# Kernel optimization log

Hardware: AMD Instinct MI355X
Metric: run time of the kernel (lower is better)

The kernel has to match this reference:

```python
import math
import jax, jax.numpy as jnp
import numpy as np

N_HEADS = 16
D_EMBED = 1024
D_HEAD = D_EMBED // N_HEADS
B, S = 4, 2048


def setup_inputs() -> dict:
    key = jax.random.key(0)
    k1, k2, k3, k4, k5 = jax.random.split(key, 5)
    scale_in = 1.0 / math.sqrt(D_EMBED)
    return {
        "x": jax.random.normal(k1, (B, S, D_EMBED), dtype=jnp.float32),
        "w_in": jax.random.normal(k2, (3 * D_EMBED, D_EMBED), dtype=jnp.float32) * scale_in,
        "b_in": jax.random.normal(k3, (3 * D_EMBED,), dtype=jnp.float32) * 0.02,
        "w_out": jax.random.normal(k4, (D_EMBED, D_EMBED), dtype=jnp.float32) * scale_in,
        "b_out": jax.random.normal(k5, (D_EMBED,), dtype=jnp.float32) * 0.02,
        "causal_mask": 1,
    }


def reference(x, w_in, b_in, w_out, b_out, causal_mask):
    Bn, Sn, D = x.shape
    # fused QKV projection (torch Linear: x @ W.T + b)
    qkv = x @ w_in.T + b_in                       # (B, S, 3D)
    q, k, v = jnp.split(qkv, 3, axis=-1)
    def to_heads(t):
        return t.reshape(Bn, Sn, N_HEADS, D_HEAD).transpose(0, 2, 1, 3)  # (B,H,S,dh)
    q, k, v = to_heads(q), to_heads(k), to_heads(v)
    # manual scaled dot-product attention, full (B,H,S,S) scores
    scores = jnp.einsum("bhqd,bhkd->bhqk", q, k)
    if causal_mask:
        tri = jnp.triu(jnp.ones((Sn, Sn), dtype=bool), k=1)
        scores = jnp.where(tri, -jnp.inf, scores)
    scores = scores / math.sqrt(D_HEAD)
    weights = jax.nn.softmax(scores, axis=-1)
    out = jnp.einsum("bhqk,bhkd->bhqd", weights, v)  # (B,H,S,dh)
    out = out.transpose(0, 2, 1, 3).reshape(Bn, Sn, D)
    return out @ w_out.T + b_out
```

## Files before the change

kernel.cpp:

```cpp
#include <hip/hip_runtime.h>

typedef __bf16 bf16x8 __attribute__((ext_vector_type(8)));
typedef float  f32x4  __attribute__((ext_vector_type(4)));
typedef unsigned int uint;

__device__ inline unsigned short f2bf(float f) {
  union { float f; unsigned int u; } v; v.f = f;
  unsigned int u = v.u;
  unsigned int r = u + 0x7FFF + ((u >> 16) & 1);
  return (unsigned short)(r >> 16);
}

__device__ inline uint pack_bf16_rhu(float a, float b) {
  uint ua = __builtin_bit_cast(uint, a) + 0x8000u;
  uint ub = __builtin_bit_cast(uint, b) + 0x8000u;
  return __builtin_amdgcn_perm(ub, ua, 0x07060302u);
}

__device__ inline void load_lds16(const unsigned short* g, unsigned short* l) {
  __builtin_amdgcn_global_load_lds(
      (const __attribute__((address_space(1))) uint*)(g),
      (__attribute__((address_space(3))) uint*)(l), 16, 0, 0);
}

__global__ void cvt_f32_bf16(const float* __restrict__ in,
                             unsigned short* __restrict__ out, int n) {
  int i = (blockIdx.x * blockDim.x + threadIdx.x) * 4;
  if (i + 3 < n) {
    float4 f = *reinterpret_cast<const float4*>(in + i);
    ushort4 o;
    o.x = f2bf(f.x); o.y = f2bf(f.y); o.z = f2bf(f.z); o.w = f2bf(f.w);
    *reinterpret_cast<ushort4*>(out + i) = o;
  } else {
    for (; i < n; ++i) out[i] = f2bf(in[i]);
  }
}

template<bool OUT_BF16>
__global__ __launch_bounds__(256) void gemm_bt128(
    const unsigned short* __restrict__ A,
    const unsigned short* __restrict__ B,
    const float* __restrict__ bias,
    void* __restrict__ Cout,
    int M, int N, int K, int ldc, float scale, int ncut)
{
  __shared__ __attribute__((aligned(16))) unsigned short As[128 * 64];
  __shared__ __attribute__((aligned(16))) unsigned short Bs[128 * 64];

  const int t    = threadIdx.x;
  const int wave = t >> 6, lane = t & 63;
  const int l16  = lane & 15, quad = lane >> 4;
  const int wr = wave >> 1, wc = wave & 1;
  const int m0 = blockIdx.y * 128, n0 = blockIdx.x * 128;

  f32x4 acc[4][4] = {};

  for (int k0 = 0; k0 < K; k0 += 64) {
#pragma unroll
    for (int i = 0; i < 4; ++i) {
      int chunk = i * 256 + t;
      int row = chunk >> 3, col = (chunk & 7) * 8;
      load_lds16(A + (size_t)(m0 + row) * K + k0 + col, As + chunk * 8);
    }
#pragma unroll
    for (int i = 0; i < 4; ++i) {
      int chunk = i * 256 + t;
      int row = chunk >> 3, col = (chunk & 7) * 8;
      load_lds16(B + (size_t)(n0 + row) * K + k0 + col, Bs + chunk * 8);
    }
    __syncthreads();
#pragma unroll
    for (int ks = 0; ks < 2; ++ks) {
      bf16x8 af[4], bfr[4];
#pragma unroll
      for (int mt = 0; mt < 4; ++mt)
        af[mt] = *(const bf16x8*)(As + (wr * 64 + mt * 16 + l16) * 64 + ks * 32 + quad * 8);
#pragma unroll
      for (int nt = 0; nt < 4; ++nt)
        bfr[nt] = *(const bf16x8*)(Bs + (wc * 64 + nt * 16 + l16) * 64 + ks * 32 + quad * 8);
#pragma unroll
      for (int mt = 0; mt < 4; ++mt)
#pragma unroll
        for (int nt = 0; nt < 4; ++nt)
          acc[mt][nt] = __builtin_amdgcn_mfma_f32_16x16x32_bf16(af[mt], bfr[nt], acc[mt][nt], 0, 0, 0);
    }
    __syncthreads();
  }

#pragma unroll
  for (int nt = 0; nt < 4; ++nt) {
    int col = n0 + wc * 64 + nt * 16 + l16;
    float bv = bias[col];
    float mlt = (col < ncut) ? scale : 1.0f;
#pragma unroll
    for (int mt = 0; mt < 4; ++mt) {
#pragma unroll
      for (int r = 0; r < 4; ++r) {
        int row = m0 + wr * 64 + mt * 16 + quad * 4 + r;
        float v = (acc[mt][nt][r] + bv) * mlt;
        if (OUT_BF16)
          ((unsigned short*)Cout)[(size_t)row * ldc + col] = f2bf(v);
        else
          ((float*)Cout)[(size_t)row * ldc + col] = v;
      }
    }
  }
}

__global__ __launch_bounds__(256) void attn(
    const unsigned short* __restrict__ qkv,
    unsigned short* __restrict__ y,
    const int* __restrict__ flag)
{
  __shared__ __attribute__((aligned(16))) unsigned short Qs[64][72];
  __shared__ __attribute__((aligned(16))) unsigned short Ks[64][72];
  __shared__ __attribute__((aligned(16))) unsigned short VtF[64 * 64];

  const int t    = threadIdx.x;
  const int wave = t >> 6, lane = t & 63;
  const int l16  = lane & 15, quad = lane >> 4;
  const int idx = blockIdx.x;
  const int bh  = idx & 63;
  const int qt  = 31 - (idx >> 6);
  const int b = bh >> 4, h = bh & 15;
  const int causal = flag[0];
  const int q0 = qt * 64;

  const unsigned short* Qg = qkv + (size_t)b * 2048 * 3072 + h * 64;
  const unsigned short* Kg = Qg + 1024;
  const unsigned short* Vg = Qg + 2048;

  {
    int r = t >> 2, c = (t & 3) * 16;
    const unsigned short* src = Qg + (size_t)(q0 + r) * 3072 + c;
    *(uint4*)&Qs[r][c]     = *(const uint4*)src;
    *(uint4*)&Qs[r][c + 8] = *(const uint4*)(src + 8);
  }
  __syncthreads();
  bf16x8 qf[2];
  qf[0] = *(const bf16x8*)&Qs[wave * 16 + l16][quad * 8];
  qf[1] = *(const bf16x8*)&Qs[wave * 16 + l16][32 + quad * 8];
  __syncthreads();
  unsigned short (*Ps)[72] = Qs;

  f32x4 ot[4] = {};
  float l_lane = 0.f;
  const int q_glob = q0 + wave * 16 + l16;
  const int jmax = causal ? qt : 31;
  const int h7 = ((l16 >> 3) + (l16 & 7)) & 7;

  const int kr = t >> 2, kc = (t & 3) * 16;
  const int vr = t >> 3, vg = t & 7, vc = vg * 8;
  const int bk0 = vr >> 3, r7 = vr & 7;

  uint4 kreg0, kreg1, vreg0, vreg1;
  {
    const unsigned short* src = Kg + (size_t)kr * 3072 + kc;
    kreg0 = *(const uint4*)src;
    kreg1 = *(const uint4*)(src + 8);
    vreg0 = *(const uint4*)(Vg + (size_t)vr * 3072 + vc);
    vreg1 = *(const uint4*)(Vg + (size_t)(vr + 32) * 3072 + vc);
  }

  for (int j = 0; j <= jmax; ++j) {
    *(uint4*)&Ks[kr][kc]     = kreg0;
    *(uint4*)&Ks[kr][kc + 8] = kreg1;
    {
      const unsigned short* vs0 = (const unsigned short*)&vreg0;
      const unsigned short* vs1 = (const unsigned short*)&vreg1;
#pragma unroll
      for (int i = 0; i < 8; ++i) {
        int d = vc + i;
        VtF[d * 64 + (((bk0     + vg + i) & 7) << 3) + r7] = vs0[i];
        VtF[d * 64 + (((bk0 + 4 + vg + i) & 7) << 3) + r7] = vs1[i];
      }
    }
    __syncthreads();

    if (j < jmax) {
      const int kvn = (j + 1) * 64;
      const unsigned short* src = Kg + (size_t)(kvn + kr) * 3072 + kc;
      kreg0 = *(const uint4*)src;
      kreg1 = *(const uint4*)(src + 8);
      vreg0 = *(const uint4*)(Vg + (size_t)(kvn + vr) * 3072 + vc);
      vreg1 = *(const uint4*)(Vg + (size_t)(kvn + vr + 32) * 3072 + vc);
    }

    f32x4 st[4] = {};
#pragma unroll
    for (int ks = 0; ks < 2; ++ks) {
#pragma unroll
      for (int mt = 0; mt < 4; ++mt) {
        bf16x8 kf = *(const bf16x8*)&Ks[mt * 16 + l16][ks * 32 + quad * 8];
        st[mt] = __builtin_amdgcn_mfma_f32_16x16x32_bf16(kf, qf[ks], st[mt], 0, 0, 0);
      }
    }

    const bool diag = (causal != 0) && (j == qt);
    const int kv0 = j * 64;
#pragma unroll
    for (int mt = 0; mt < 4; ++mt) {
      float p[4];
#pragma unroll
      for (int r = 0; r < 4; ++r) {
        float pv = __builtin_amdgcn_exp2f(st[mt][r]);
        if (diag) {
          int kv = kv0 + mt * 16 + quad * 4 + r;
          if (kv > q_glob) pv = 0.f;
        }
        p[r] = pv;
      }
      l_lane += (p[0] + p[1]) + (p[2] + p[3]);
      uint2 w;
      w.x = pack_bf16_rhu(p[0], p[1]);
      w.y = pack_bf16_rhu(p[2], p[3]);
      *(uint2*)&Ps[wave * 16 + l16][mt * 16 + quad * 4] = w;
    }
    __threadfence_block();

#pragma unroll
    for (int ks = 0; ks < 2; ++ks) {
      bf16x8 pf = *(const bf16x8*)&Ps[wave * 16 + l16][ks * 32 + quad * 8];
#pragma unroll
      for (int mt = 0; mt < 4; ++mt) {
        int blk = (ks * 4 + quad + 2 * mt + h7) & 7;
        bf16x8 vf = *(const bf16x8*)(VtF + (mt * 16 + l16) * 64 + (blk << 3));
        ot[mt] = __builtin_amdgcn_mfma_f32_16x16x32_bf16(vf, pf, ot[mt], 0, 0, 0);
      }
    }
    __syncthreads();
  }

  l_lane += __shfl_xor(l_lane, 16);
  l_lane += __shfl_xor(l_lane, 32);
  float inv = 1.f / l_lane;

#pragma unroll
  for (int mt = 0; mt < 4; ++mt) {
    uint2 w;
    w.x = pack_bf16_rhu(ot[mt][0] * inv, ot[mt][1] * inv);
    w.y = pack_bf16_rhu(ot[mt][2] * inv, ot[mt][3] * inv);
    *(uint2*)&Ps[wave * 16 + l16][mt * 16 + quad * 4] = w;
  }
  __syncthreads();
  {
    int r = t >> 2, c = (t & 3) * 16;
    size_t base = ((size_t)b * 2048 + q0 + r) * 1024 + h * 64 + c;
    *(uint4*)(y + base)     = *(const uint4*)&Ps[r][c];
    *(uint4*)(y + base + 8) = *(const uint4*)&Ps[r][c + 8];
  }
}

extern "C" void kernel_launch(void* const* d_in, const int* in_sizes, int n_in,
                              void* d_out, int out_size, void* d_ws, size_t ws_size,
                              hipStream_t stream) {
  const float* x     = (const float*)d_in[0];
  const float* w_in  = (const float*)d_in[1];
  const float* b_in  = (const float*)d_in[2];
  const float* w_out = (const float*)d_in[3];
  const float* b_out = (const float*)d_in[4];
  const int*   cmask = (const int*)d_in[5];

  char* ws = (char*)d_ws;
  unsigned short* x_bf     = (unsigned short*)(ws);
  unsigned short* w_in_bf  = (unsigned short*)(ws + 16777216);
  unsigned short* w_out_bf = (unsigned short*)(ws + 23068672);
  unsigned short* qkv_bf   = (unsigned short*)(ws + 25165824);
  unsigned short* y_bf     = (unsigned short*)(ws + 75497472);

  const int n1 = 8192 * 1024, n2 = 3072 * 1024, n3 = 1024 * 1024;
  cvt_f32_bf16<<<dim3((n1 / 4 + 255) / 256), 256, 0, stream>>>(x, x_bf, n1);
  cvt_f32_bf16<<<dim3((n2 / 4 + 255) / 256), 256, 0, stream>>>(w_in, w_in_bf, n2);
  cvt_f32_bf16<<<dim3((n3 / 4 + 255) / 256), 256, 0, stream>>>(w_out, w_out_bf, n3);

  gemm_bt128<true><<<dim3(24, 64), 256, 0, stream>>>(
      x_bf, w_in_bf, b_in, qkv_bf, 8192, 3072, 1024, 3072,
      0.18033688011112042f, 1024);

  attn<<<dim3(2048), 256, 0, stream>>>(qkv_bf, y_bf, cmask);

  gemm_bt128<false><<<dim3(8, 64), 256, 0, stream>>>(
      y_bf, w_out_bf, b_out, d_out, 8192, 1024, 1024, 1024, 1.0f, 0);
}
```

Measured before the change: 282.2 us.

## Fuse conversions, XOR-swizzle GEMM LDS tiles, pre-transpose V for attention

```diff
diff --git a/kernel.cpp b/kernel.cpp
--- a/kernel.cpp
+++ b/kernel.cpp
@@ -23,17 +23,23 @@
       (__attribute__((address_space(3))) uint*)(l), 16, 0, 0);
 }
 
-__global__ void cvt_f32_bf16(const float* __restrict__ in,
-                             unsigned short* __restrict__ out, int n) {
+__device__ inline void cvt4(const float* in, unsigned short* out) {
+  float4 f = *reinterpret_cast<const float4*>(in);
+  ushort4 o;
+  o.x = f2bf(f.x); o.y = f2bf(f.y); o.z = f2bf(f.z); o.w = f2bf(f.w);
+  *reinterpret_cast<ushort4*>(out) = o;
+}
+
+__global__ void cvt_all(const float* __restrict__ x, const float* __restrict__ w_in,
+                        const float* __restrict__ w_out,
+                        unsigned short* __restrict__ x_bf,
+                        unsigned short* __restrict__ w_in_bf,
+                        unsigned short* __restrict__ w_out_bf) {
+  const int n1 = 8192 * 1024, n2 = 3072 * 1024;
   int i = (blockIdx.x * blockDim.x + threadIdx.x) * 4;
-  if (i + 3 < n) {
-    float4 f = *reinterpret_cast<const float4*>(in + i);
-    ushort4 o;
-    o.x = f2bf(f.x); o.y = f2bf(f.y); o.z = f2bf(f.z); o.w = f2bf(f.w);
-    *reinterpret_cast<ushort4*>(out + i) = o;
-  } else {
-    for (; i < n; ++i) out[i] = f2bf(in[i]);
-  }
+  if (i < n1)            cvt4(x + i, x_bf + i);
+  else if (i < n1 + n2)  cvt4(w_in + (i - n1), w_in_bf + (i - n1));
+  else                   cvt4(w_out + (i - n1 - n2), w_out_bf + (i - n1 - n2));
 }
 
 template<bool OUT_BF16>
@@ -52,6 +58,7 @@
   const int l16  = lane & 15, quad = lane >> 4;
   const int wr = wave >> 1, wc = wave & 1;
   const int m0 = blockIdx.y * 128, n0 = blockIdx.x * 128;
+  const int l8 = l16 & 7;
 
   f32x4 acc[4][4] = {};
 
@@ -59,14 +66,16 @@
 #pragma unroll
     for (int i = 0; i < 4; ++i) {
       int chunk = i * 256 + t;
-      int row = chunk >> 3, col = (chunk & 7) * 8;
-      load_lds16(A + (size_t)(m0 + row) * K + k0 + col, As + chunk * 8);
+      int row = chunk >> 3, cb = chunk & 7;
+      int gcb = cb ^ (row & 7);
+      load_lds16(A + (size_t)(m0 + row) * K + k0 + gcb * 8, As + chunk * 8);
     }
 #pragma unroll
     for (int i = 0; i < 4; ++i) {
       int chunk = i * 256 + t;
-      int row = chunk >> 3, col = (chunk & 7) * 8;
-      load_lds16(B + (size_t)(n0 + row) * K + k0 + col, Bs + chunk * 8);
+      int row = chunk >> 3, cb = chunk & 7;
+      int gcb = cb ^ (row & 7);
+      load_lds16(B + (size_t)(n0 + row) * K + k0 + gcb * 8, Bs + chunk * 8);
     }
     __syncthreads();
 #pragma unroll
@@ -74,10 +83,12 @@
       bf16x8 af[4], bfr[4];
 #pragma unroll
       for (int mt = 0; mt < 4; ++mt)
-        af[mt] = *(const bf16x8*)(As + (wr * 64 + mt * 16 + l16) * 64 + ks * 32 + quad * 8);
+        af[mt] = *(const bf16x8*)(As + (wr * 64 + mt * 16 + l16) * 64 +
+                                  (((ks * 4 + quad) ^ l8) << 3));
 #pragma unroll
       for (int nt = 0; nt < 4; ++nt)
-        bfr[nt] = *(const bf16x8*)(Bs + (wc * 64 + nt * 16 + l16) * 64 + ks * 32 + quad * 8);
+        bfr[nt] = *(const bf16x8*)(Bs + (wc * 64 + nt * 16 + l16) * 64 +
+                                   (((ks * 4 + quad) ^ l8) << 3));
 #pragma unroll
       for (int mt = 0; mt < 4; ++mt)
 #pragma unroll
@@ -107,8 +118,33 @@
   }
 }
 
+__global__ __launch_bounds__(256) void vtrans(const unsigned short* __restrict__ qkv,
+                                              unsigned short* __restrict__ vt) {
+  __shared__ unsigned short Ls[64][72];
+  const int t = threadIdx.x;
+  const int s0 = blockIdx.x * 64;
+  const int bh = blockIdx.y, b = bh >> 4, h = bh & 15;
+  {
+    int s = t >> 2, c = (t & 3) * 16;
+    const unsigned short* src = qkv + ((size_t)(b * 2048 + s0 + s)) * 3072 + 2048 + h * 64 + c;
+    *(uint4*)&Ls[s][c]     = *(const uint4*)src;
+    *(uint4*)&Ls[s][c + 8] = *(const uint4*)(src + 8);
+  }
+  __syncthreads();
+  {
+    int d = t >> 2, sb = (t & 3) * 16;
+    unsigned short tmp[16];
+#pragma unroll
+    for (int i = 0; i < 16; ++i) tmp[i] = Ls[sb + i][d];
+    size_t base = ((size_t)bh * 64 + d) * 2048 + s0 + sb;
+    *(uint4*)(vt + base)     = *(const uint4*)tmp;
+    *(uint4*)(vt + base + 8) = *(const uint4*)(tmp + 8);
+  }
+}
+
 __global__ __launch_bounds__(256) void attn(
     const unsigned short* __restrict__ qkv,
+    const unsigned short* __restrict__ vt,
     unsigned short* __restrict__ y,
     const int* __restrict__ flag)
 {
@@ -128,7 +164,7 @@
 
   const unsigned short* Qg = qkv + (size_t)b * 2048 * 3072 + h * 64;
   const unsigned short* Kg = Qg + 1024;
-  const unsigned short* Vg = Qg + 2048;
+  const unsigned short* Vtg = vt + (size_t)bh * 64 * 2048;
 
   {
     int r = t >> 2, c = (t & 3) * 16;
@@ -147,34 +183,27 @@
   float l_lane = 0.f;
   const int q_glob = q0 + wave * 16 + l16;
   const int jmax = causal ? qt : 31;
-  const int h7 = ((l16 >> 3) + (l16 & 7)) & 7;
 
   const int kr = t >> 2, kc = (t & 3) * 16;
-  const int vr = t >> 3, vg = t & 7, vc = vg * 8;
-  const int bk0 = vr >> 3, r7 = vr & 7;
+  const int vd = t >> 2, vb = t & 3;
+  const int vpos0 = ((vb     + vd) & 7) << 3;
+  const int vpos1 = ((vb + 4 + vd) & 7) << 3;
+  const unsigned short* vrow = Vtg + (size_t)vd * 2048;
 
   uint4 kreg0, kreg1, vreg0, vreg1;
   {
     const unsigned short* src = Kg + (size_t)kr * 3072 + kc;
     kreg0 = *(const uint4*)src;
     kreg1 = *(const uint4*)(src + 8);
-    vreg0 = *(const uint4*)(Vg + (size_t)vr * 3072 + vc);
-    vreg1 = *(const uint4*)(Vg + (size_t)(vr + 32) * 3072 + vc);
+    vreg0 = *(const uint4*)(vrow + vb * 8);
+    vreg1 = *(const uint4*)(vrow + vb * 8 + 32);
   }
 
   for (int j = 0; j <= jmax; ++j) {
     *(uint4*)&Ks[kr][kc]     = kreg0;
     *(uint4*)&Ks[kr][kc + 8] = kreg1;
-    {
-      const unsigned short* vs0 = (const unsigned short*)&vreg0;
-      const unsigned short* vs1 = (const unsigned short*)&vreg1;
-#pragma unroll
-      for (int i = 0; i < 8; ++i) {
-        int d = vc + i;
-        VtF[d * 64 + (((bk0     + vg + i) & 7) << 3) + r7] = vs0[i];
-        VtF[d * 64 + (((bk0 + 4 + vg + i) & 7) << 3) + r7] = vs1[i];
-      }
-    }
+    *(uint4*)(VtF + vd * 64 + vpos0) = vreg0;
+    *(uint4*)(VtF + vd * 64 + vpos1) = vreg1;
     __syncthreads();
 
     if (j < jmax) {
@@ -182,8 +211,8 @@
       const unsigned short* src = Kg + (size_t)(kvn + kr) * 3072 + kc;
       kreg0 = *(const uint4*)src;
       kreg1 = *(const uint4*)(src + 8);
-      vreg0 = *(const uint4*)(Vg + (size_t)(kvn + vr) * 3072 + vc);
-      vreg1 = *(const uint4*)(Vg + (size_t)(kvn + vr + 32) * 3072 + vc);
+      vreg0 = *(const uint4*)(vrow + kvn + vb * 8);
+      vreg1 = *(const uint4*)(vrow + kvn + vb * 8 + 32);
     }
 
     f32x4 st[4] = {};
@@ -223,8 +252,8 @@
       bf16x8 pf = *(const bf16x8*)&Ps[wave * 16 + l16][ks * 32 + quad * 8];
 #pragma unroll
       for (int mt = 0; mt < 4; ++mt) {
-        int blk = (ks * 4 + quad + 2 * mt + h7) & 7;
-        bf16x8 vf = *(const bf16x8*)(VtF + (mt * 16 + l16) * 64 + (blk << 3));
+        int pos = ((ks * 4 + quad + l16) & 7) << 3;
+        bf16x8 vf = *(const bf16x8*)(VtF + (mt * 16 + l16) * 64 + pos);
         ot[mt] = __builtin_amdgcn_mfma_f32_16x16x32_bf16(vf, pf, ot[mt], 0, 0, 0);
       }
     }
@@ -267,17 +296,18 @@
   unsigned short* w_out_bf = (unsigned short*)(ws + 23068672);
   unsigned short* qkv_bf   = (unsigned short*)(ws + 25165824);
   unsigned short* y_bf     = (unsigned short*)(ws + 75497472);
-
-  const int n1 = 8192 * 1024, n2 = 3072 * 1024, n3 = 1024 * 1024;
-  cvt_f32_bf16<<<dim3((n1 / 4 + 255) / 256), 256, 0, stream>>>(x, x_bf, n1);
-  cvt_f32_bf16<<<dim3((n2 / 4 + 255) / 256), 256, 0, stream>>>(w_in, w_in_bf, n2);
-  cvt_f32_bf16<<<dim3((n3 / 4 + 255) / 256), 256, 0, stream>>>(w_out, w_out_bf, n3);
+  unsigned short* vt_bf    = x_bf;
+
+  const int ntot = (8192 + 3072 + 1024) * 1024;
+  cvt_all<<<dim3(ntot / 4 / 256), 256, 0, stream>>>(x, w_in, w_out, x_bf, w_in_bf, w_out_bf);
 
   gemm_bt128<true><<<dim3(24, 64), 256, 0, stream>>>(
       x_bf, w_in_bf, b_in, qkv_bf, 8192, 3072, 1024, 3072,
       0.18033688011112042f, 1024);
 
-  attn<<<dim3(2048), 256, 0, stream>>>(qkv_bf, y_bf, cmask);
+  vtrans<<<dim3(32, 64), 256, 0, stream>>>(qkv_bf, vt_bf);
+
+  attn<<<dim3(2048), 256, 0, stream>>>(qkv_bf, vt_bf, y_bf, cmask);
 
   gemm_bt128<false><<<dim3(8, 64), 256, 0, stream>>>(
       y_bf, w_out_bf, b_out, d_out, 8192, 1024, 1024, 1024, 1.0f, 0);
```

Measured after the change: 262.2 us. -7.1%, faster.
